# Kernel tuning notes

Measured on AMD Instinct MI355X. Metric: run time of the kernel, lower is better.

The kernel has to match this reference:

```python
import jax, jax.numpy as jnp
import numpy as np

DT = 1.0
SEQ, BATCH, HID = 2048, 512, 256

def setup_inputs() -> dict:
    key = jax.random.key(0)
    ks = jax.random.split(key, 4)
    x = jax.random.normal(ks[0], (SEQ, BATCH, 1), dtype=jnp.float32)
    # small init scale keeps tanh unsaturated and the Euler recurrence stable
    W1 = 0.3 * jax.random.normal(ks[1], (2, HID), dtype=jnp.float32)
    b1 = jnp.zeros((HID,), jnp.float32)
    W2 = (0.3 / np.sqrt(HID)) * jax.random.normal(ks[2], (HID, HID), dtype=jnp.float32)
    b2 = jnp.zeros((HID,), jnp.float32)
    W3 = (0.1 / np.sqrt(HID)) * jax.random.normal(ks[3], (HID, 1), dtype=jnp.float32)
    b3 = jnp.zeros((1,), jnp.float32)
    state0 = jnp.zeros((BATCH,), jnp.float32)
    return {"x": x, "W1": W1, "b1": b1, "W2": W2, "b2": b2, "W3": W3, "b3": b3, "state0": state0}

def reference(x, W1, b1, W2, b2, W3, b3, state0):
    # Forward-Euler ODE integration: y[n+1] = y[n] + dt * f(x[n], y[n]).
    # Torch code returns odeint_output[:-1, :, None], i.e. the state at each
    # step BEFORE the update, with shape identical to x.
    xs = x[:, :, 0]  # (seq, batch) -- derivative_network.input = x.squeeze(2)

    def f(x_t, y):
        u = jnp.stack([x_t, y], axis=-1)          # (B, 2)
        h = jnp.tanh(u @ W1 + b1)                 # (B, H)
        h = jnp.tanh(h @ W2 + b2)                 # (B, H)
        return (h @ W3 + b3)[:, 0]                # (B,)

    def step(state, x_t):
        new_state = state + DT * f(x_t, state)
        return new_state, state                   # emit pre-update state

    _, ys = jax.lax.scan(step, state0, xs)        # ys: (seq, batch)
    return ys[:, :, None]                         # (seq, batch, 1), same shape as x
```

## Files before the change

kernel.cpp:

```cpp
#include <hip/hip_runtime.h>


#define SEQ 2048
#define BATCH 512
#define HID 256
#define LDA 288

typedef __bf16 bf16x8 __attribute__((ext_vector_type(8)));
typedef short short8 __attribute__((ext_vector_type(8)));
typedef float f32x4 __attribute__((ext_vector_type(4)));

__device__ __forceinline__ unsigned short f2bf_rne(float f) {
  unsigned u = __builtin_bit_cast(unsigned, f);
  u += 0x7fffu + ((u >> 16) & 1u);
  return (unsigned short)(u >> 16);
}

__device__ __forceinline__ float tanh_e(float x) {
  float t = __builtin_amdgcn_exp2f(x * 2.8853900817779268f);
  return __builtin_fmaf(-2.f, __builtin_amdgcn_rcpf(t + 1.f), 1.f);
}

__device__ __forceinline__ float row16_sum_to_lane15(float v) {
  int s;
  s = __builtin_amdgcn_update_dpp(0, __builtin_bit_cast(int, v), 0x111, 0xf, 0xf, true);
  v += __builtin_bit_cast(float, s);
  s = __builtin_amdgcn_update_dpp(0, __builtin_bit_cast(int, v), 0x112, 0xf, 0xf, true);
  v += __builtin_bit_cast(float, s);
  s = __builtin_amdgcn_update_dpp(0, __builtin_bit_cast(int, v), 0x114, 0xf, 0xf, true);
  v += __builtin_bit_cast(float, s);
  s = __builtin_amdgcn_update_dpp(0, __builtin_bit_cast(int, v), 0x118, 0xf, 0xf, true);
  v += __builtin_bit_cast(float, s);
  return v;
}

__global__ void pack_w2_kernel(const float* __restrict__ W2,
                               unsigned short* __restrict__ ws) {
  int idx = blockIdx.x * 256 + threadIdx.x;
  int e    = idx & 7;
  int l    = (idx >> 3) & 63;
  int kc   = (idx >> 9) & 7;
  int tile = idx >> 12;
  int k = kc * 32 + (l >> 4) * 8 + e;
  int c = tile * 16 + (l & 15);
  ws[idx] = f2bf_rne(W2[k * HID + c]);
}

__global__ __launch_bounds__(512, 2) void odenet_kernel(
    const float* __restrict__ x, const float* __restrict__ W1,
    const float* __restrict__ b1, const unsigned short* __restrict__ wsW2,
    const float* __restrict__ b2, const float* __restrict__ W3,
    const float* __restrict__ b3, const float* __restrict__ state0,
    float* __restrict__ out) {
  __shared__ __align__(16) unsigned short A_lds[2 * LDA];
  __shared__ __align__(16) float partial[2][8];
  __shared__ __align__(16) float2 x_lds[SEQ];
  __shared__ __align__(16) float2 y_lds[SEQ];

  const int tid  = threadIdx.x;
  const int lane = tid & 63;
  const int wave = tid >> 6;
  const int rh   = tid >> 8;
  const int j    = tid & 255;
  const int b0   = blockIdx.x * 2;

  const float w10 = W1[j];
  const float w11 = W1[HID + j];
  const float b1j = b1[j];
  const float b3v = b3[0];
  const int c0 = wave * 32 + (lane & 15);
  const int c1 = c0 + 16;
  const float b2c0 = b2[c0], w3c0 = W3[c0];
  const float b2c1 = b2[c1], w3c1 = W3[c1];

  short8 bf0[8], bf1[8];
  {
    const short8* wp = (const short8*)wsW2;
    const int t0 = wave * 2;
#pragma unroll
    for (int kc = 0; kc < 8; ++kc) {
      bf0[kc] = wp[((t0    ) * 8 + kc) * 64 + lane];
      bf1[kc] = wp[((t0 + 1) * 8 + kc) * 64 + lane];
    }
  }

  {
    const float* xg = x + b0;
#pragma unroll
    for (int k = 0; k < 4; ++k) {
      const int t = tid + k * 512;
      x_lds[t] = *(const float2*)&xg[t * BATCH];
    }
  }

  const int aoff = ((lane >> 2) & 1) * LDA + (lane >> 4) * 8;

  const f32x4 kZero = {0.f, 0.f, 0.f, 0.f};

  const float2 y_init = *(const float2*)&state0[b0];
  float y_own = rh ? y_init.y : y_init.x;

  if (tid < 16) ((float*)partial)[tid] = -0.125f * b3v;
  __syncthreads();

  {
    const float2 x0 = x_lds[0];
    const float xv = rh ? x0.y : x0.x;
    const float xa0 = __builtin_fmaf(xv, w10, b1j);
    const float T0 = tanh_e(__builtin_fmaf(b3v, w11, __builtin_fmaf(y_own, w11, xa0)));
  }
  float2 xr0 = x_lds[0];
  float T, E;
  {
    const float xv = rh ? xr0.y : xr0.x;
    const float xa0 = __builtin_fmaf(xv, w10, b1j);
    T = tanh_e(__builtin_fmaf(b3v, w11, __builtin_fmaf(y_own, w11, xa0)));
    E = w11 * __builtin_fmaf(-T, T, 1.f);
  }

  for (int t = 0; t < SEQ; ++t) {
    const f32x4 qa = *(const f32x4*)&partial[rh][0];
    const f32x4 qb = *(const f32x4*)&partial[rh][4];
    const float s_own = ((qa[0] + qa[1]) + (qa[2] + qa[3])) +
                        ((qb[0] + qb[1]) + (qb[2] + qb[3]));
    A_lds[rh * LDA + j] = f2bf_rne(__builtin_fmaf(s_own, E, T));
    __syncthreads();

    const float2 xr = x_lds[(t + 1 < SEQ) ? t + 1 : t];

    short8 areg[8];
#pragma unroll
    for (int kc = 0; kc < 8; ++kc)
      areg[kc] = *(const short8*)&A_lds[aoff + kc * 32];

    f32x4 acc0, acc1;
    {
      const bf16x8 a = __builtin_bit_cast(bf16x8, areg[0]);
      acc0 = __builtin_amdgcn_mfma_f32_16x16x32_bf16(a, __builtin_bit_cast(bf16x8, bf0[0]), kZero, 0, 0, 0);
      acc1 = __builtin_amdgcn_mfma_f32_16x16x32_bf16(a, __builtin_bit_cast(bf16x8, bf1[0]), kZero, 0, 0, 0);
    }
#pragma unroll
    for (int kc = 1; kc < 8; ++kc) {
      const bf16x8 a = __builtin_bit_cast(bf16x8, areg[kc]);
      acc0 = __builtin_amdgcn_mfma_f32_16x16x32_bf16(a, __builtin_bit_cast(bf16x8, bf0[kc]), acc0, 0, 0, 0);
      acc1 = __builtin_amdgcn_mfma_f32_16x16x32_bf16(a, __builtin_bit_cast(bf16x8, bf1[kc]), acc1, 0, 0, 0);
    }

    y_own += s_own + b3v;
    if (j == 0) ((float*)&y_lds[t])[rh] = y_own;
    {
      const float xv = rh ? xr.y : xr.x;
      const float xaN = __builtin_fmaf(xv, w10, b1j);
      T = tanh_e(__builtin_fmaf(b3v, w11, __builtin_fmaf(y_own, w11, xaN)));
      E = w11 * __builtin_fmaf(-T, T, 1.f);
    }

    const float s = tanh_e(acc0[0] + b2c0) * w3c0 +
                    tanh_e(acc1[0] + b2c1) * w3c1;
    const float r = row16_sum_to_lane15(s);
    if ((lane & 15) == 15 && lane < 32)
      partial[lane >> 4][wave] = r;
    __syncthreads();
  }

#pragma unroll
  for (int k = 0; k < 4; ++k) {
    const int t = tid + k * 512;
    *(float2*)&out[t * BATCH + b0] = y_lds[t];
  }
}

extern "C" void kernel_launch(void* const* d_in, const int* in_sizes, int n_in,
                              void* d_out, int out_size, void* d_ws, size_t ws_size,
                              hipStream_t stream) {
  const float* x  = (const float*)d_in[0];
  const float* W1 = (const float*)d_in[1];
  const float* b1 = (const float*)d_in[2];
  const float* W2 = (const float*)d_in[3];
  const float* b2 = (const float*)d_in[4];
  const float* W3 = (const float*)d_in[5];
  const float* b3 = (const float*)d_in[6];
  const float* s0 = (const float*)d_in[7];
  unsigned short* ws = (unsigned short*)d_ws;
  float* out = (float*)d_out;

  pack_w2_kernel<<<256, 256, 0, stream>>>(W2, ws);
  odenet_kernel<<<256, 512, 0, stream>>>(x, W1, b1, ws, b2, W3, b3, s0, out);
}
```

Measured before the change: 1.190 ms.

## Split hidden linearization into T and E GEMM rows, one barrier per step

The first-layer activation is linearized as T + s*E, and both T and E rows now go through the MFMA (four A rows instead of two), so the layer-2 product for the current s is rebuilt after the GEMM with a cross-lane shuffle and FMA. The LDS buffers for A and the partial sums are double-buffered, which removes the second __syncthreads per time step. The s reduction moves after the MFMA so it overlaps with matrix work. The cost is twice the A rows, extra shuffles, and dropping the two-blocks-per-CU occupancy hint.

Result: slower. 1.400 ms (+17.7%).

```diff
diff --git a/kernel.cpp b/kernel.cpp
--- a/kernel.cpp
+++ b/kernel.cpp
@@ -4,7 +4,7 @@
 #define SEQ 2048
 #define BATCH 512
 #define HID 256
-#define LDA 288
+#define LDA 264
 
 typedef __bf16 bf16x8 __attribute__((ext_vector_type(8)));
 typedef short short8 __attribute__((ext_vector_type(8)));
@@ -46,14 +46,14 @@
   ws[idx] = f2bf_rne(W2[k * HID + c]);
 }
 
-__global__ __launch_bounds__(512, 2) void odenet_kernel(
+__global__ __launch_bounds__(512, 1) void odenet_kernel(
     const float* __restrict__ x, const float* __restrict__ W1,
     const float* __restrict__ b1, const unsigned short* __restrict__ wsW2,
     const float* __restrict__ b2, const float* __restrict__ W3,
     const float* __restrict__ b3, const float* __restrict__ state0,
     float* __restrict__ out) {
-  __shared__ __align__(16) unsigned short A_lds[2 * LDA];
-  __shared__ __align__(16) float partial[2][8];
+  __shared__ __align__(16) unsigned short A_lds[2][4 * LDA];
+  __shared__ __align__(16) float partial[2][2][8];
   __shared__ __align__(16) float2 x_lds[SEQ];
   __shared__ __align__(16) float2 y_lds[SEQ];
 
@@ -93,45 +93,36 @@
     }
   }
 
-  const int aoff = ((lane >> 2) & 1) * LDA + (lane >> 4) * 8;
+  const int aoff = ((lane >> 2) & 3) * LDA + (lane >> 4) * 8;
 
   const f32x4 kZero = {0.f, 0.f, 0.f, 0.f};
 
   const float2 y_init = *(const float2*)&state0[b0];
   float y_own = rh ? y_init.y : y_init.x;
 
-  if (tid < 16) ((float*)partial)[tid] = -0.125f * b3v;
-  __syncthreads();
+  if (tid < 16) partial[1][tid >> 3][tid & 7] = -0.125f * b3v;
 
-  {
-    const float2 x0 = x_lds[0];
-    const float xv = rh ? x0.y : x0.x;
-    const float xa0 = __builtin_fmaf(xv, w10, b1j);
-    const float T0 = tanh_e(__builtin_fmaf(b3v, w11, __builtin_fmaf(y_own, w11, xa0)));
-  }
-  float2 xr0 = x_lds[0];
   float T, E;
   {
-    const float xv = rh ? xr0.y : xr0.x;
+    const float2 x0 = *(const float2*)&x[b0];
+    const float xv = rh ? x0.y : x0.x;
     const float xa0 = __builtin_fmaf(xv, w10, b1j);
     T = tanh_e(__builtin_fmaf(b3v, w11, __builtin_fmaf(y_own, w11, xa0)));
     E = w11 * __builtin_fmaf(-T, T, 1.f);
   }
+  __syncthreads();
 
   for (int t = 0; t < SEQ; ++t) {
-    const f32x4 qa = *(const f32x4*)&partial[rh][0];
-    const f32x4 qb = *(const f32x4*)&partial[rh][4];
-    const float s_own = ((qa[0] + qa[1]) + (qa[2] + qa[3])) +
-                        ((qb[0] + qb[1]) + (qb[2] + qb[3]));
-    A_lds[rh * LDA + j] = f2bf_rne(__builtin_fmaf(s_own, E, T));
+    const int buf = t & 1;
+    A_lds[buf][rh * LDA + j]       = f2bf_rne(T);
+    A_lds[buf][(2 + rh) * LDA + j] = f2bf_rne(E);
     __syncthreads();
 
-    const float2 xr = x_lds[(t + 1 < SEQ) ? t + 1 : t];
-
+    const unsigned short* ab = &A_lds[buf][0];
     short8 areg[8];
 #pragma unroll
     for (int kc = 0; kc < 8; ++kc)
-      areg[kc] = *(const short8*)&A_lds[aoff + kc * 32];
+      areg[kc] = *(const short8*)&ab[aoff + kc * 32];
 
     f32x4 acc0, acc1;
     {
@@ -146,21 +137,36 @@
       acc1 = __builtin_amdgcn_mfma_f32_16x16x32_bf16(a, __builtin_bit_cast(bf16x8, bf1[kc]), acc1, 0, 0, 0);
     }
 
+    const f32x4 q0a = *(const f32x4*)&partial[buf ^ 1][0][0];
+    const f32x4 q0b = *(const f32x4*)&partial[buf ^ 1][0][4];
+    const f32x4 q1a = *(const f32x4*)&partial[buf ^ 1][1][0];
+    const f32x4 q1b = *(const f32x4*)&partial[buf ^ 1][1][4];
+    const float s0sum = ((q0a[0] + q0a[1]) + (q0a[2] + q0a[3])) +
+                        ((q0b[0] + q0b[1]) + (q0b[2] + q0b[3]));
+    const float s1sum = ((q1a[0] + q1a[1]) + (q1a[2] + q1a[3])) +
+                        ((q1b[0] + q1b[1]) + (q1b[2] + q1b[3]));
+
+    const float s_own = rh ? s1sum : s0sum;
     y_own += s_own + b3v;
     if (j == 0) ((float*)&y_lds[t])[rh] = y_own;
     {
+      const float2 xr = x_lds[(t + 1 < SEQ) ? t + 1 : t];
       const float xv = rh ? xr.y : xr.x;
       const float xaN = __builtin_fmaf(xv, w10, b1j);
       T = tanh_e(__builtin_fmaf(b3v, w11, __builtin_fmaf(y_own, w11, xaN)));
       E = w11 * __builtin_fmaf(-T, T, 1.f);
     }
 
-    const float s = tanh_e(acc0[0] + b2c0) * w3c0 +
-                    tanh_e(acc1[0] + b2c1) * w3c1;
-    const float r = row16_sum_to_lane15(s);
+    const float s_lane = ((lane >> 4) & 1) ? s1sum : s0sum;
+    const float e0 = __shfl_xor(acc0[0], 32, 64);
+    const float e1 = __shfl_xor(acc1[0], 32, 64);
+    const float h0 = __builtin_fmaf(s_lane, e0, acc0[0]);
+    const float h1v = __builtin_fmaf(s_lane, e1, acc1[0]);
+    const float sres = tanh_e(h0 + b2c0) * w3c0 +
+                       tanh_e(h1v + b2c1) * w3c1;
+    const float r = row16_sum_to_lane15(sres);
     if ((lane & 15) == 15 && lane < 32)
-      partial[lane >> 4][wave] = r;
-    __syncthreads();
+      partial[buf][lane >> 4][wave] = r;
   }
 
 #pragma unroll
```
